# Kernel optimization log

Measured on AMD Instinct MI355X. Metric: run time of the kernel, lower is better.

Reference implementation:

```python
import jax, jax.numpy as jnp
import numpy as np

B, H, W, C = 8, 64, 64, 64
DI = 2 * C   # d_inner = ssm_ratio * hidden_dim
N = 1        # ssm_d_state
K = 4        # scan directions
R = 4        # dt_rank = ceil(C/16)
EPS = 1e-5


def _ln(x, w, b):
    mu = x.mean(-1, keepdims=True)
    var = x.var(-1, keepdims=True)
    return (x - mu) / jnp.sqrt(var + EPS) * w + b


def _vss(x, p):
    (norm1_w, norm1_b, in_proj_w, conv_w, x_proj_w, dt_projs_w, dt_projs_b,
     A_logs, Ds, out_norm_w, out_norm_b, out_proj_w, norm2_w, norm2_b,
     fc1_w, fc1_b, fc2_w, fc2_b) = p
    # ---- SS2D branch (forward_type='v2') ----
    h = _ln(x, norm1_w, norm1_b)
    xz = h @ in_proj_w.T                      # (B,H,W,2*DI)
    xc, z = jnp.split(xz, 2, axis=-1)
    z = jax.nn.silu(z)
    xc = xc.transpose(0, 3, 1, 2)             # (B,DI,H,W)
    xc = jax.lax.conv_general_dilated(
        xc, conv_w, (1, 1), [(1, 1), (1, 1)], feature_group_count=DI,
        dimension_numbers=('NCHW', 'OIHW', 'NCHW'))  # depthwise 3x3, no bias
    xc = jax.nn.silu(xc)
    L = H * W
    # CrossScan: row-major, col-major, and their reverses
    x0 = xc.reshape(B, DI, L)
    x1 = xc.transpose(0, 1, 3, 2).reshape(B, DI, L)
    xs = jnp.stack([x0, x1, x0[..., ::-1], x1[..., ::-1]], axis=1)  # (B,K,DI,L)
    x_dbl = jnp.einsum('bkdl,kcd->bkcl', xs, x_proj_w)
    dts, Bs, Cs = x_dbl[:, :, :R], x_dbl[:, :, R:R + N], x_dbl[:, :, R + N:]
    delta = jax.nn.softplus(jnp.einsum('bkrl,kdr->bkdl', dts, dt_projs_w)
                            + dt_projs_b[None, :, :, None])          # (B,K,DI,L)
    A = -jnp.exp(A_logs).reshape(K, DI, N)
    # diagonal linear recurrence h_t = a_t*h_{t-1} + b_t via associative scan
    a = jnp.exp(delta[..., None] * A[None, :, :, None, :])           # (B,K,DI,L,N)
    b = delta[..., None] * Bs.transpose(0, 1, 3, 2)[:, :, None] * xs[..., None]
    def comb(c1, c2):
        a1, b1 = c1
        a2, b2 = c2
        return a1 * a2, b1 * a2 + b2
    _, hst = jax.lax.associative_scan(comb, (a, b), axis=3)          # (B,K,DI,L,N)
    ys = jnp.einsum('bkdln,bknl->bkdl', hst, Cs) \
         + Ds.reshape(K, DI)[None, :, :, None] * xs
    # CrossMerge
    ys = ys[:, :2] + ys[:, 2:, :, ::-1]
    y = ys[:, 0] + ys[:, 1].reshape(B, DI, W, H).transpose(0, 1, 3, 2).reshape(B, DI, L)
    y = y.transpose(0, 2, 1).reshape(B, H, W, DI)
    y = _ln(y, out_norm_w, out_norm_b)
    y = (y * z) @ out_proj_w.T
    x = x + y
    # ---- MLP branch ----
    h2 = _ln(x, norm2_w, norm2_b)
    h2 = jax.nn.gelu(h2 @ fc1_w.T + fc1_b, approximate=False)
    return x + (h2 @ fc2_w.T + fc2_b)


def setup_inputs():
    key = jax.random.key(0)
    ks = jax.random.split(key, 16)
    g = lambda i, shape, s=0.02: jax.random.normal(ks[i], shape, jnp.float32) * s
    return {
        'mag': jax.random.normal(ks[0], (B, H, W, C), jnp.float32),
        'phase': jax.random.normal(ks[1], (B, H, W, C), jnp.float32),
        'norm1_w': jnp.ones((2, C)), 'norm1_b': jnp.zeros((2, C)),
        'in_proj_w': g(2, (2, 2 * DI, C)),
        'conv_w': g(3, (2, DI, 1, 3, 3), 0.1),
        'x_proj_w': g(4, (2, K, R + 2 * N, DI)),
        'dt_projs_w': g(5, (2, K, DI, R), 0.1),
        'dt_projs_b': g(6, (2, K, DI), 0.1),
        'A_logs': g(7, (2, K * DI, N), 1.0),
        'Ds': jnp.ones((2, K * DI)),
        'out_norm_w': jnp.ones((2, DI)), 'out_norm_b': jnp.zeros((2, DI)),
        'out_proj_w': g(8, (2, C, DI)),
        'norm2_w': jnp.ones((2, C)), 'norm2_b': jnp.zeros((2, C)),
        'fc1_w': g(9, (2, 4 * C, C)), 'fc1_b': jnp.zeros((2, 4 * C)),
        'fc2_w': g(10, (2, C, 4 * C)), 'fc2_b': jnp.zeros((2, C)),
    }


def reference(mag, phase, norm1_w, norm1_b, in_proj_w, conv_w, x_proj_w,
              dt_projs_w, dt_projs_b, A_logs, Ds, out_norm_w, out_norm_b,
              out_proj_w, norm2_w, norm2_b, fc1_w, fc1_b, fc2_w, fc2_b):
    params = (norm1_w, norm1_b, in_proj_w, conv_w, x_proj_w, dt_projs_w,
              dt_projs_b, A_logs, Ds, out_norm_w, out_norm_b, out_proj_w,
              norm2_w, norm2_b, fc1_w, fc1_b, fc2_w, fc2_b)
    outs = jax.vmap(_vss)(jnp.stack([mag, phase]), params)  # branch dim = 2
    s = outs[0] + outs[1]
    return (s, s)
```

## Files before the change

kernel.cpp:

```cpp
#include <hip/hip_runtime.h>
#include <math.h>

#define LL   4096
#define DI   128
#define CC   64
#define BB   8
#define KK   4
#define LB   32768
#define NPIX 2097152
#define EPSF 1e-5f

#define OFF_XCIN   ((size_t)0)
#define OFF_XCONV  ((size_t)4194304)
#define OFF_XCONVT ((size_t)8388608)
#define OFF_Z      ((size_t)12582912)
#define OFF_Y      ((size_t)16777216)
#define OFF_YT     ((size_t)20971520)
#define OFF_XDBL   ((size_t)25165824)
#define ISTRIDE    ((size_t)25952256)
#define OFF_YCOMBT OFF_XCIN
#define OFF_XNEW   OFF_YT
#define OFF_SB     OFF_Y

typedef short v8s __attribute__((ext_vector_type(8)));
typedef float v4f __attribute__((ext_vector_type(4)));

__device__ __forceinline__ float fexp_(float x){ return __expf(x); }
__device__ __forceinline__ float silu_(float x){ return __fdividef(x, 1.f+__expf(-x)); }
__device__ __forceinline__ float softplusf_(float x){
  return fmaxf(x,0.f) + __logf(1.f + __expf(-fabsf(x)));
}
__device__ __forceinline__ float geluf_(float x){ return 0.5f*x*(1.f+erff(x*0.70710678118f)); }
__device__ __forceinline__ short bf16_(float x){
  unsigned u = __float_as_uint(x);
  u += 0x7FFF + ((u>>16)&1);
  return (short)(u>>16);
}
__device__ __forceinline__ float bf2f_(short s){
  return __uint_as_float(((unsigned)(unsigned short)s)<<16);
}

#define LD16(dst, ptr) { const float4* p4_=(const float4*)(ptr);                 \
  float4 v0_=p4_[0], v1_=p4_[1], v2_=p4_[2], v3_=p4_[3];                         \
  dst[0]=v0_.x; dst[1]=v0_.y; dst[2]=v0_.z; dst[3]=v0_.w;                        \
  dst[4]=v1_.x; dst[5]=v1_.y; dst[6]=v1_.z; dst[7]=v1_.w;                        \
  dst[8]=v2_.x; dst[9]=v2_.y; dst[10]=v2_.z; dst[11]=v2_.w;                      \
  dst[12]=v3_.x; dst[13]=v3_.y; dst[14]=v3_.z; dst[15]=v3_.w; }
#define LD16H(dst, ptr) { const v8s* p8_=(const v8s*)(ptr);                      \
  v8s a0_=p8_[0], a1_=p8_[1];                                                    \
  _Pragma("unroll") for(int e_=0;e_<8;++e_){ dst[e_]=bf2f_(a0_[e_]);             \
                                             dst[8+e_]=bf2f_(a1_[e_]); } }
#define LD16HR(dst, ptr) { const v8s* p8_=(const v8s*)(ptr);                     \
  v8s a0_=p8_[0], a1_=p8_[1];                                                    \
  _Pragma("unroll") for(int e_=0;e_<8;++e_){ dst[15-e_]=bf2f_(a0_[e_]);          \
                                             dst[7-e_]=bf2f_(a1_[e_]); } }
#define ST16H(ptr, srcv) { v8s o0_, o1_;                                         \
  _Pragma("unroll") for(int e_=0;e_<8;++e_){ o0_[e_]=bf16_(srcv[e_]);            \
                                             o1_[e_]=bf16_(srcv[8+e_]); }        \
  ((v8s*)(ptr))[0]=o0_; ((v8s*)(ptr))[1]=o1_; }

__global__ __launch_bounds__(256) void k1_ln_inproj(
    const float* __restrict__ xmag, const float* __restrict__ xph,
    const float* __restrict__ n1w_, const float* __restrict__ n1b_,
    const float* __restrict__ ipw_, float* __restrict__ ws)
{
  const int i = blockIdx.y;
  const float* xin = i ? xph : xmag;
  const float* n1w = n1w_ + i*CC;
  const float* n1b = n1b_ + i*CC;
  const float* ipw = ipw_ + i*2*DI*CC;
  float* base = ws + (size_t)i*ISTRIDE;
  const int t = threadIdx.x, lane = t & 63;
  const int wv = __builtin_amdgcn_readfirstlane(t >> 6);
  const int m = lane & 15, quad = lane >> 4;
  const int p0 = blockIdx.x*64;
  const int b = p0 >> 12, l0 = p0 & (LL-1);

  __shared__ short hlds[64*72];
  __shared__ short w1lds[128*72];
  __shared__ float outs[128*68];

  {
    float hn[CC];
    const float* xr = xin + (size_t)(p0 + lane)*CC;
    LD16(hn, xr); LD16((hn+16), xr+16); LD16((hn+32), xr+32); LD16((hn+48), xr+48);
    float s1=0.f, s2=0.f;
    #pragma unroll
    for(int c=0;c<CC;++c){ s1 += hn[c]; s2 += hn[c]*hn[c]; }
    const float mu = s1*(1.f/CC);
    const float rs = rsqrtf(s2*(1.f/CC) - mu*mu + EPSF);
    if(wv==0){
      #pragma unroll
      for(int q=0;q<8;++q){
        v8s s;
        #pragma unroll
        for(int e=0;e<8;++e){
          const int c = q*8+e;
          s[e] = bf16_((hn[c]-mu)*rs*n1w[c] + n1b[c]);
        }
        *(v8s*)&hlds[lane*72 + q*8] = s;
      }
    }
  }

  for(int h=0; h<2; ++h){
    if(h) __syncthreads();
    {
      const int jl = t >> 1, hc = (t & 1)*32;
      const float* src = ipw + (size_t)(h*128 + jl)*64 + hc;
      #pragma unroll
      for(int q=0;q<4;++q){
        const float4 fa = ((const float4*)src)[q*2];
        const float4 fb = ((const float4*)src)[q*2+1];
        v8s s;
        s[0]=bf16_(fa.x); s[1]=bf16_(fa.y); s[2]=bf16_(fa.z); s[3]=bf16_(fa.w);
        s[4]=bf16_(fb.x); s[5]=bf16_(fb.y); s[6]=bf16_(fb.z); s[7]=bf16_(fb.w);
        *(v8s*)&w1lds[jl*72 + hc + q*8] = s;
      }
    }
    __syncthreads();
    #pragma unroll 2
    for(int nt=0; nt<8; ++nt){
      v4f acc = (v4f){0.f,0.f,0.f,0.f};
      #pragma unroll
      for(int ks=0; ks<2; ++ks){
        const v8s a = *(const v8s*)&hlds[(wv*16 + m)*72 + ks*32 + quad*8];
        const v8s bb = *(const v8s*)&w1lds[(nt*16 + m)*72 + ks*32 + quad*8];
        acc = __builtin_amdgcn_mfma_f32_16x16x32_bf16(a, bb, acc, 0, 0, 0);
      }
      *(float4*)&outs[(nt*16 + m)*68 + wv*16 + quad*4] =
          make_float4(acc[0], acc[1], acc[2], acc[3]);
    }
    __syncthreads();
    const int jl = t >> 1, hc = (t & 1)*32;
    if(h==0){
      short* xcb = (short*)(base + OFF_XCIN) + (size_t)b*DI*LL + (size_t)jl*LL + l0 + hc;
      const float* so = &outs[jl*68 + hc];
      ST16H(xcb, so);
      ST16H(xcb+16, (so+16));
    } else {
      short* zr = (short*)(base + OFF_Z) + (size_t)jl*LB + p0 + hc;
      float tmp[32];
      #pragma unroll
      for(int e=0;e<32;++e) tmp[e] = silu_(outs[jl*68 + hc + e]);
      ST16H(zr, tmp);
      ST16H(zr+16, (tmp+16));
    }
  }
}

__global__ __launch_bounds__(256) void k2_dwconv(
    const float* __restrict__ cw_, float* __restrict__ ws)
{
  const int i = blockIdx.y;
  const int bd = blockIdx.x;
  const int d = bd & (DI-1);
  const float* cw = cw_ + i*DI*9 + d*9;
  const short* xcin = (const short*)(ws + (size_t)i*ISTRIDE + OFF_XCIN) + (size_t)bd*LL;
  short* xconv  = (short*)(ws + (size_t)i*ISTRIDE + OFF_XCONV ) + (size_t)bd*LL;
  short* xconvT = (short*)(ws + (size_t)i*ISTRIDE + OFF_XCONVT) + (size_t)bd*LL;
  __shared__ float tin[64*65];
  __shared__ float tout[64*65];
  const int t = threadIdx.x;
  float w9[9];
  #pragma unroll
  for(int q=0;q<9;++q) w9[q] = cw[q];
  for(int idx=t; idx<4096; idx+=256)
    tin[(idx>>6)*65 + (idx&63)] = bf2f_(xcin[idx]);
  __syncthreads();
  const int w = t & 63, hb = (t>>6)*16;
  #pragma unroll
  for(int r=0;r<16;++r){
    const int h = hb + r;
    float acc = 0.f;
    #pragma unroll
    for(int dy=0;dy<3;++dy){
      const int hh = h + dy - 1;
      if(hh>=0 && hh<64){
        #pragma unroll
        for(int dx=0;dx<3;++dx){
          const int ww = w + dx - 1;
          if(ww>=0 && ww<64) acc += tin[hh*65+ww]*w9[dy*3+dx];
        }
      }
    }
    const float o = silu_(acc);
    tout[h*65+w] = o;
    xconv[h*64+w] = bf16_(o);
  }
  __syncthreads();
  const int hcol = t & 63, wb = (t>>6)*16;
  #pragma unroll
  for(int r=0;r<16;++r){
    const int wp = wb + r;
    xconvT[wp*64 + hcol] = bf16_(tout[hcol*65 + wp]);
  }
}

__global__ __launch_bounds__(256) void k3a_xproj(
    const float* __restrict__ xpw_, float* __restrict__ ws)
{
  const int i = blockIdx.z;
  const int b = blockIdx.y >> 1;
  const int kp = blockIdx.y & 1;
  const int l = blockIdx.x*256 + threadIdx.x;
  const short* src = (const short*)(ws + (size_t)i*ISTRIDE + (kp? OFF_XCONVT : OFF_XCONV))
                     + (size_t)b*DI*LL;
  const float* xpwF = xpw_ + i*KK*6*DI + kp*6*DI;
  const float* xpwB = xpw_ + i*KK*6*DI + (kp+2)*6*DI;
  float accF[6] = {0,0,0,0,0,0};
  float accB[6] = {0,0,0,0,0,0};
  for(int d=0; d<DI; ++d){
    const float xv = bf2f_(src[(size_t)d*LL + l]);
    #pragma unroll
    for(int c=0;c<6;++c){
      accF[c] += xv * xpwF[c*DI + d];
      accB[c] += xv * xpwB[c*DI + d];
    }
  }
  short* xdF = (short*)(ws + (size_t)i*ISTRIDE + OFF_XDBL) + (size_t)(b*KK+kp  )*6*LL;
  short* xdB = (short*)(ws + (size_t)i*ISTRIDE + OFF_XDBL) + (size_t)(b*KK+kp+2)*6*LL;
  #pragma unroll
  for(int c=0;c<6;++c) xdF[(size_t)c*LL + l] = bf16_(accF[c]);
  #pragma unroll
  for(int c=0;c<6;++c) xdB[(size_t)c*LL + (LL-1-l)] = bf16_(accB[c]);
}

__global__ __launch_bounds__(256,3) void k3b_scan(
    const float* __restrict__ dtw_, const float* __restrict__ dtb_,
    const float* __restrict__ alog_, const float* __restrict__ Ds_,
    float* __restrict__ ws)
{
  const int gid = blockIdx.x;
  const int i = blockIdx.y;
  const int d  = gid & (DI-1);
  const int b  = gid >> 7;
  const int t = threadIdx.x, lane = t & 63, wv = t >> 6;
  float* base = ws + (size_t)i*ISTRIDE;
  const int l0 = t*16;
  const int s0 = LL - 16 - l0;

  __shared__ float tile[64*65];
  __shared__ float wAg[4], wBg[4], vAg[4], vBg[4];

  #pragma unroll 1
  for(int kp=0; kp<2; ++kp){
    const short* src = (const short*)(base + (kp? OFF_XCONVT : OFF_XCONV)) + (size_t)(b*DI+d)*LL;
    const short* xdF = (const short*)(base + OFF_XDBL) + (size_t)(b*KK+kp  )*6*LL;
    const short* xdB = (const short*)(base + OFF_XDBL) + (size_t)(b*KK+kp+2)*6*LL;
    const int kdF = kp*DI + d, kdB = (kp+2)*DI + d;
    const float4 wF = ((const float4*)dtw_)[i*KK*DI + kdF];
    const float4 wB = ((const float4*)dtw_)[i*KK*DI + kdB];
    const float biasF = dtb_[i*KK*DI + kdF], biasB = dtb_[i*KK*DI + kdB];
    const float AvF = -fexp_(alog_[i*KK*DI + kdF]);
    const float AvB = -fexp_(alog_[i*KK*DI + kdB]);
    const float Dsum = Ds_[i*KK*DI + kdF] + Ds_[i*KK*DI + kdB];

    float vX[16], aF[16], bF[16], aB[16], bB[16];
    float fA = 1.f, fB = 0.f, gA = 1.f, gB = 0.f;
    LD16H(vX, src + l0);

    {
      float pre[16], r0[16];
      LD16H(r0, xdF + 0*LL + l0);
      #pragma unroll
      for(int j=0;j<16;++j) pre[j] = biasF + wF.x*r0[j];
      LD16H(r0, xdF + 1*LL + l0);
      #pragma unroll
      for(int j=0;j<16;++j) pre[j] += wF.y*r0[j];
      LD16H(r0, xdF + 2*LL + l0);
      #pragma unroll
      for(int j=0;j<16;++j) pre[j] += wF.z*r0[j];
      LD16H(r0, xdF + 3*LL + l0);
      #pragma unroll
      for(int j=0;j<16;++j) pre[j] += wF.w*r0[j];
      LD16H(r0, xdF + 4*LL + l0);
      #pragma unroll
      for(int j=0;j<16;++j){
        const float delta = softplusf_(pre[j]);
        aF[j] = fexp_(delta*AvF);
        bF[j] = delta*r0[j]*vX[j];
        fB = fB*aF[j] + bF[j];
        fA *= aF[j];
      }
    }
    {
      float pre[16], r0[16];
      LD16HR(r0, xdB + 0*LL + s0);
      #pragma unroll
      for(int j=0;j<16;++j) pre[j] = biasB + wB.x*r0[j];
      LD16HR(r0, xdB + 1*LL + s0);
      #pragma unroll
      for(int j=0;j<16;++j) pre[j] += wB.y*r0[j];
      LD16HR(r0, xdB + 2*LL + s0);
      #pragma unroll
      for(int j=0;j<16;++j) pre[j] += wB.z*r0[j];
      LD16HR(r0, xdB + 3*LL + s0);
      #pragma unroll
      for(int j=0;j<16;++j) pre[j] += wB.w*r0[j];
      LD16HR(r0, xdB + 4*LL + s0);
      #pragma unroll
      for(int j=15;j>=0;--j){
        const float delta = softplusf_(pre[j]);
        aB[j] = fexp_(delta*AvB);
        bB[j] = delta*r0[j]*vX[j];
        gB = gB*aB[j] + bB[j];
        gA *= aB[j];
      }
    }

    #pragma unroll
    for(int off=1; off<64; off<<=1){
      const float aL = __shfl_up(fA, off);
      const float bL = __shfl_up(fB, off);
      if(lane >= off){ fB = bL*fA + fB; fA = aL*fA; }
    }
    float pA = __shfl_up(fA, 1), pB = __shfl_up(fB, 1);
    if(lane==0){ pA=1.f; pB=0.f; }
    #pragma unroll
    for(int off=1; off<64; off<<=1){
      const float aR = __shfl_down(gA, off);
      const float bR = __shfl_down(gB, off);
      if(lane + off < 64){ gB = gA*bR + gB; gA = gA*aR; }
    }
    float qA = __shfl_down(gA, 1), qB = __shfl_down(gB, 1);
    if(lane==63){ qA=1.f; qB=0.f; }

    if(kp) __syncthreads();
    if(lane==63){ wAg[wv]=fA; wBg[wv]=fB; }
    if(lane==0){ vAg[wv]=gA; vBg[wv]=gB; }
    __syncthreads();
    float eB=0.f;
    for(int u=0; u<wv; ++u){ eB = wAg[u]*eB + wBg[u]; }
    float rB=0.f;
    for(int u=3; u>wv; --u){ rB = vAg[u]*rB + vBg[u]; }

    float hf = pA*eB + pB;
    float hb = qA*rB + qB;

    float out[16], cc[16];
    LD16H(cc, xdF + 5*LL + l0);
    #pragma unroll
    for(int j=0;j<16;++j){
      hf = aF[j]*hf + bF[j];
      out[j] = hf*cc[j] + Dsum*vX[j];
    }
    LD16HR(cc, xdB + 5*LL + s0);
    #pragma unroll
    for(int j=15;j>=0;--j){
      hb = aB[j]*hb + bB[j];
      out[j] += hb*cc[j];
    }

    if(kp==0){
      #pragma unroll
      for(int j=0;j<16;++j){
        const int l = l0 + j;
        tile[(l>>6)*65 + (l&63)] = out[j];
      }
    } else {
      #pragma unroll
      for(int j=0;j<16;++j){
        const int q = l0 + j;
        tile[(q&63)*65 + (q>>6)] += out[j];
      }
    }
  }

  __syncthreads();
  {
    short* ycT = (short*)(base + OFF_YCOMBT);
    float o[16];
    #pragma unroll
    for(int j=0;j<16;++j)
      o[j] = tile[(t>>2)*65 + (t&3)*16 + j];
    ST16H(ycT + (size_t)d*LB + b*LL + l0, o);
  }
}

__global__ __launch_bounds__(256) void k4a_proj(
    const float* __restrict__ xmag, const float* __restrict__ xph,
    const float* __restrict__ onw_, const float* __restrict__ onb_,
    const float* __restrict__ opw_, float* __restrict__ ws)
{
  const int i = blockIdx.y;
  const float* xin = i ? xph : xmag;
  const float* onw = onw_ + i*DI;
  const float* onb = onb_ + i*DI;
  const float* opw = opw_ + i*CC*DI;
  float* base = ws + (size_t)i*ISTRIDE;
  const short* ycT = (const short*)(base + OFF_YCOMBT);
  const short* zT  = (const short*)(base + OFF_Z);
  const int t = threadIdx.x, lane = t & 63;
  const int wv = __builtin_amdgcn_readfirstlane(t >> 6);
  const int m = lane & 15, quad = lane >> 4;
  const int p0 = blockIdx.x*64;
  const int p = p0 + lane;

  __shared__ short ynlds[64*136];
  __shared__ short wlds[64*136];
  __shared__ float st[64][9];

  float yv[32];
  float s1=0.f, s2=0.f;
  #pragma unroll 8
  for(int c=0;c<32;++c){
    const float v = bf2f_(ycT[(size_t)(wv*32+c)*LB + p]);
    yv[c]=v; s1+=v; s2+=v*v;
  }
  st[lane][wv*2]=s1; st[lane][wv*2+1]=s2;
  __syncthreads();
  const float S1 = st[lane][0]+st[lane][2]+st[lane][4]+st[lane][6];
  const float S2 = st[lane][1]+st[lane][3]+st[lane][5]+st[lane][7];
  const float mu = S1*(1.f/DI);
  const float rs = rsqrtf(S2*(1.f/DI) - mu*mu + EPSF);
  #pragma unroll
  for(int cq=0;cq<8;++cq){
    short4 s4;
    #pragma unroll
    for(int e=0;e<4;++e){
      const int c = cq*4+e;
      const int d = wv*32 + c;
      ((short*)&s4)[e] = bf16_(((yv[c]-mu)*rs*onw[d] + onb[d]) * bf2f_(zT[(size_t)d*LB + p]));
    }
    *(short4*)&ynlds[lane*136 + wv*32 + cq*4] = s4;
  }
  {
    const int ol = t >> 2, seg = (t & 3)*32;
    const float* src = opw + (size_t)ol*DI + seg;
    #pragma unroll
    for(int q=0;q<4;++q){
      const float4 fa = ((const float4*)src)[q*2];
      const float4 fb = ((const float4*)src)[q*2+1];
      v8s s;
      s[0]=bf16_(fa.x); s[1]=bf16_(fa.y); s[2]=bf16_(fa.z); s[3]=bf16_(fa.w);
      s[4]=bf16_(fb.x); s[5]=bf16_(fb.y); s[6]=bf16_(fb.z); s[7]=bf16_(fb.w);
      *(v8s*)&wlds[ol*136 + seg + q*8] = s;
    }
  }
  __syncthreads();

  v4f accs[4];
  #pragma unroll
  for(int nt=0; nt<4; ++nt){
    v4f acc = (v4f){0.f,0.f,0.f,0.f};
    #pragma unroll
    for(int ks=0; ks<4; ++ks){
      const v8s a = *(const v8s*)&ynlds[(wv*16 + m)*136 + ks*32 + quad*8];
      const v8s b = *(const v8s*)&wlds[(nt*16 + m)*136 + ks*32 + quad*8];
      acc = __builtin_amdgcn_mfma_f32_16x16x32_bf16(a, b, acc, 0, 0, 0);
    }
    accs[nt] = acc;
  }
  short* xnew = (short*)(base + OFF_XNEW);
  #pragma unroll
  for(int nt=0; nt<4; ++nt){
    #pragma unroll
    for(int r=0;r<4;++r){
      const int pp = p0 + wv*16 + quad*4 + r;
      const int o = nt*16 + m;
      xnew[(size_t)pp*CC + o] = bf16_(accs[nt][r] + xin[(size_t)pp*CC + o]);
    }
  }
}

__global__ __launch_bounds__(256) void k4b_mlp(
    const float* __restrict__ n2w_, const float* __restrict__ n2b_,
    const float* __restrict__ f1w_, const float* __restrict__ f1b_,
    const float* __restrict__ f2w_, const float* __restrict__ f2b_,
    float* __restrict__ ws)
{
  const int i = blockIdx.y;
  const float* n2w = n2w_ + i*CC;
  const float* n2b = n2b_ + i*CC;
  const float* f1w = f1w_ + i*256*64;
  const float* f1b = f1b_ + i*256;
  const float* f2w = f2w_ + i*64*256;
  const float* f2b = f2b_ + i*CC;
  float* base = ws + (size_t)i*ISTRIDE;
  const short* xnew = (const short*)(base + OFF_XNEW);
  const int t = threadIdx.x, lane = t & 63;
  const int wv = __builtin_amdgcn_readfirstlane(t >> 6);
  const int m = lane & 15, quad = lane >> 4;
  const int p0 = blockIdx.x*64;

  __shared__ short hlds[64*72];
  __shared__ short w1lds[128*72];
  __shared__ short glds[64*136];
  __shared__ short w2lds[64*136];

  {
    float h2[64];
    const short* xr = xnew + (size_t)(p0 + lane)*CC;
    LD16H(h2, xr); LD16H((h2+16), xr+16); LD16H((h2+32), xr+32); LD16H((h2+48), xr+48);
    float s1=0.f, s2=0.f;
    #pragma unroll
    for(int c=0;c<CC;++c){ s1 += h2[c]; s2 += h2[c]*h2[c]; }
    const float mu = s1*(1.f/CC);
    const float rs = rsqrtf(s2*(1.f/CC) - mu*mu + EPSF);
    if(wv==0){
      #pragma unroll
      for(int q=0;q<8;++q){
        v8s s;
        #pragma unroll
        for(int e=0;e<8;++e){
          const int c = q*8+e;
          s[e] = bf16_((h2[c]-mu)*rs*n2w[c] + n2b[c]);
        }
        *(v8s*)&hlds[lane*72 + q*8] = s;
      }
    }
  }

  v4f acc2[4];
  #pragma unroll
  for(int n=0;n<4;++n) acc2[n] = (v4f){0.f,0.f,0.f,0.f};

  for(int h=0; h<2; ++h){
    if(h) __syncthreads();
    {
      const int jl = t >> 1, hc = (t & 1)*32;
      const float* src = f1w + (size_t)(h*128 + jl)*64 + hc;
      #pragma unroll
      for(int q=0;q<4;++q){
        const float4 fa = ((const float4*)src)[q*2];
        const float4 fb = ((const float4*)src)[q*2+1];
        v8s s;
        s[0]=bf16_(fa.x); s[1]=bf16_(fa.y); s[2]=bf16_(fa.z); s[3]=bf16_(fa.w);
        s[4]=bf16_(fb.x); s[5]=bf16_(fb.y); s[6]=bf16_(fb.z); s[7]=bf16_(fb.w);
        *(v8s*)&w1lds[jl*72 + hc + q*8] = s;
      }
    }
    {
      const int ol = t >> 2, seg = (t & 3)*32;
      const float* src = f2w + (size_t)ol*256 + h*128 + seg;
      #pragma unroll
      for(int q=0;q<4;++q){
        const float4 fa = ((const float4*)src)[q*2];
        const float4 fb = ((const float4*)src)[q*2+1];
        v8s s;
        s[0]=bf16_(fa.x); s[1]=bf16_(fa.y); s[2]=bf16_(fa.z); s[3]=bf16_(fa.w);
        s[4]=bf16_(fb.x); s[5]=bf16_(fb.y); s[6]=bf16_(fb.z); s[7]=bf16_(fb.w);
        *(v8s*)&w2lds[ol*136 + seg + q*8] = s;
      }
    }
    __syncthreads();
    #pragma unroll 2
    for(int nt=0; nt<8; ++nt){
      v4f acc = (v4f){0.f,0.f,0.f,0.f};
      #pragma unroll
      for(int ks=0; ks<2; ++ks){
        const v8s a = *(const v8s*)&hlds[(wv*16 + m)*72 + ks*32 + quad*8];
        const v8s b = *(const v8s*)&w1lds[(nt*16 + m)*72 + ks*32 + quad*8];
        acc = __builtin_amdgcn_mfma_f32_16x16x32_bf16(a, b, acc, 0, 0, 0);
      }
      const float bj = f1b[h*128 + nt*16 + m];
      #pragma unroll
      for(int r=0;r<4;++r){
        glds[(wv*16 + quad*4 + r)*136 + nt*16 + m] = bf16_(geluf_(acc[r] + bj));
      }
    }
    #pragma unroll
    for(int nt=0; nt<4; ++nt){
      v4f acc = acc2[nt];
      #pragma unroll
      for(int ks=0; ks<4; ++ks){
        const v8s a = *(const v8s*)&glds[(wv*16 + m)*136 + ks*32 + quad*8];
        const v8s b = *(const v8s*)&w2lds[(nt*16 + m)*136 + ks*32 + quad*8];
        acc = __builtin_amdgcn_mfma_f32_16x16x32_bf16(a, b, acc, 0, 0, 0);
      }
      acc2[nt] = acc;
    }
  }

  short* sb = (short*)(base + OFF_SB);
  #pragma unroll
  for(int nt=0; nt<4; ++nt){
    const float bo = f2b[nt*16 + m];
    #pragma unroll
    for(int r=0;r<4;++r){
      const int p = p0 + wv*16 + quad*4 + r;
      const int o = nt*16 + m;
      sb[(size_t)p*CC + o] = bf16_(acc2[nt][r] + bo + bf2f_(xnew[(size_t)p*CC + o]));
    }
  }
}

__global__ __launch_bounds__(256) void k5_final(
    const float* __restrict__ ws, float* __restrict__ out)
{
  const int idx = blockIdx.x*256 + threadIdx.x;
  const v8s a = ((const v8s*)(ws + OFF_SB))[idx];
  const v8s b = ((const v8s*)(ws + ISTRIDE + OFF_SB))[idx];
  float4 v0, v1;
  v0.x = bf2f_(a[0])+bf2f_(b[0]); v0.y = bf2f_(a[1])+bf2f_(b[1]);
  v0.z = bf2f_(a[2])+bf2f_(b[2]); v0.w = bf2f_(a[3])+bf2f_(b[3]);
  v1.x = bf2f_(a[4])+bf2f_(b[4]); v1.y = bf2f_(a[5])+bf2f_(b[5]);
  v1.z = bf2f_(a[6])+bf2f_(b[6]); v1.w = bf2f_(a[7])+bf2f_(b[7]);
  ((float4*)out)[idx*2]   = v0;
  ((float4*)out)[idx*2+1] = v1;
  ((float4*)out)[NPIX/4 + idx*2]   = v0;
  ((float4*)out)[NPIX/4 + idx*2+1] = v1;
}

extern "C" void kernel_launch(void* const* d_in, const int* in_sizes, int n_in,
                              void* d_out, int out_size, void* d_ws, size_t ws_size,
                              hipStream_t stream)
{
  const float* mag  = (const float*)d_in[0];
  const float* ph   = (const float*)d_in[1];
  const float* n1w  = (const float*)d_in[2];
  const float* n1b  = (const float*)d_in[3];
  const float* ipw  = (const float*)d_in[4];
  const float* cw   = (const float*)d_in[5];
  const float* xpw  = (const float*)d_in[6];
  const float* dtw  = (const float*)d_in[7];
  const float* dtb  = (const float*)d_in[8];
  const float* alog = (const float*)d_in[9];
  const float* Ds   = (const float*)d_in[10];
  const float* onw  = (const float*)d_in[11];
  const float* onb  = (const float*)d_in[12];
  const float* opw  = (const float*)d_in[13];
  const float* n2w  = (const float*)d_in[14];
  const float* n2b  = (const float*)d_in[15];
  const float* f1w  = (const float*)d_in[16];
  const float* f1b  = (const float*)d_in[17];
  const float* f2w  = (const float*)d_in[18];
  const float* f2b  = (const float*)d_in[19];
  float* ws = (float*)d_ws;
  float* out = (float*)d_out;

  k1_ln_inproj<<<dim3(512,2),  256, 0, stream>>>(mag, ph, n1w, n1b, ipw, ws);
  k2_dwconv   <<<dim3(1024,2), 256, 0, stream>>>(cw, ws);
  k3a_xproj   <<<dim3(16,16,2),256, 0, stream>>>(xpw, ws);
  k3b_scan    <<<dim3(1024,2), 256, 0, stream>>>(dtw, dtb, alog, Ds, ws);
  k4a_proj    <<<dim3(512,2),  256, 0, stream>>>(mag, ph, onw, onb, opw, ws);
  k4b_mlp     <<<dim3(512,2),  256, 0, stream>>>(n2w, n2b, f1w, f1b, f2w, f2b, ws);
  k5_final    <<<dim3(1024),   256, 0, stream>>>(ws, out);
}
```

Measured before the change: 282.9 us.

## Fuse out-proj, MLP and branch sum into one kernel; pre-convert weights to bf16

Merges the out-projection, residual, LayerNorm2, MLP and final branch summation into a single kernel that loops over both branches per pixel tile and writes the output directly. This removes the xnew and sb intermediate round-trips through global memory and two kernel launches. A new prep kernel converts the weights to bf16 once per call, so the GEMM kernels copy bf16 weights straight into LDS instead of converting them in every block. The trade-off is half as many blocks in the fused kernel (512 instead of 1024), each doing serial work for two branches, which may reduce parallelism. The residual is also kept in fp32 rather than rounded to bf16, a small change in numerics.

```diff
diff --git a/kernel.cpp b/kernel.cpp
--- a/kernel.cpp
+++ b/kernel.cpp
@@ -19,8 +19,12 @@
 #define OFF_XDBL   ((size_t)25165824)
 #define ISTRIDE    ((size_t)25952256)
 #define OFF_YCOMBT OFF_XCIN
-#define OFF_XNEW   OFF_YT
-#define OFF_SB     OFF_Y
+#define OFF_WB     (OFF_XDBL + (size_t)393216)
+#define WB_IPW 0
+#define WB_OPW 16384
+#define WB_F1W 24576
+#define WB_F2W 40960
+#define WB_TOT 57344
 
 typedef short v8s __attribute__((ext_vector_type(8)));
 typedef float v4f __attribute__((ext_vector_type(4)));
@@ -59,17 +63,37 @@
                                              o1_[e_]=bf16_(srcv[8+e_]); }        \
   ((v8s*)(ptr))[0]=o0_; ((v8s*)(ptr))[1]=o1_; }
 
+__global__ __launch_bounds__(256) void kw_prep(
+    const float* __restrict__ ipw_, const float* __restrict__ opw_,
+    const float* __restrict__ f1w_, const float* __restrict__ f2w_,
+    float* __restrict__ ws)
+{
+  const int i = blockIdx.y;
+  short* wb = (short*)(ws + (size_t)i*ISTRIDE + OFF_WB);
+  const int e0 = blockIdx.x*1024 + threadIdx.x;
+  #pragma unroll
+  for(int k=0;k<4;++k){
+    const int e = e0 + k*256;
+    float v;
+    if(e < WB_OPW)      v = ipw_[(size_t)i*16384 + e];
+    else if(e < WB_F1W) v = opw_[(size_t)i*8192  + (e - WB_OPW)];
+    else if(e < WB_F2W) v = f1w_[(size_t)i*16384 + (e - WB_F1W)];
+    else                v = f2w_[(size_t)i*16384 + (e - WB_F2W)];
+    wb[e] = bf16_(v);
+  }
+}
+
 __global__ __launch_bounds__(256) void k1_ln_inproj(
     const float* __restrict__ xmag, const float* __restrict__ xph,
     const float* __restrict__ n1w_, const float* __restrict__ n1b_,
-    const float* __restrict__ ipw_, float* __restrict__ ws)
+    float* __restrict__ ws)
 {
   const int i = blockIdx.y;
   const float* xin = i ? xph : xmag;
   const float* n1w = n1w_ + i*CC;
   const float* n1b = n1b_ + i*CC;
-  const float* ipw = ipw_ + i*2*DI*CC;
   float* base = ws + (size_t)i*ISTRIDE;
+  const short* wb_ipw = (const short*)(base + OFF_WB) + WB_IPW;
   const int t = threadIdx.x, lane = t & 63;
   const int wv = __builtin_amdgcn_readfirstlane(t >> 6);
   const int m = lane & 15, quad = lane >> 4;
@@ -107,16 +131,10 @@
     if(h) __syncthreads();
     {
       const int jl = t >> 1, hc = (t & 1)*32;
-      const float* src = ipw + (size_t)(h*128 + jl)*64 + hc;
-      #pragma unroll
-      for(int q=0;q<4;++q){
-        const float4 fa = ((const float4*)src)[q*2];
-        const float4 fb = ((const float4*)src)[q*2+1];
-        v8s s;
-        s[0]=bf16_(fa.x); s[1]=bf16_(fa.y); s[2]=bf16_(fa.z); s[3]=bf16_(fa.w);
-        s[4]=bf16_(fb.x); s[5]=bf16_(fb.y); s[6]=bf16_(fb.z); s[7]=bf16_(fb.w);
-        *(v8s*)&w1lds[jl*72 + hc + q*8] = s;
-      }
+      const short* src = wb_ipw + (size_t)(h*128 + jl)*64 + hc;
+      #pragma unroll
+      for(int q=0;q<4;++q)
+        *(v8s*)&w1lds[jl*72 + hc + q*8] = ((const v8s*)src)[q];
     }
     __syncthreads();
     #pragma unroll 2
@@ -378,229 +396,205 @@
   }
 }
 
-__global__ __launch_bounds__(256) void k4a_proj(
+__global__ __launch_bounds__(256) void k4_fused(
     const float* __restrict__ xmag, const float* __restrict__ xph,
     const float* __restrict__ onw_, const float* __restrict__ onb_,
-    const float* __restrict__ opw_, float* __restrict__ ws)
+    const float* __restrict__ n2w_, const float* __restrict__ n2b_,
+    const float* __restrict__ f1b_, const float* __restrict__ f2b_,
+    float* __restrict__ ws, float* __restrict__ out)
 {
-  const int i = blockIdx.y;
-  const float* xin = i ? xph : xmag;
-  const float* onw = onw_ + i*DI;
-  const float* onb = onb_ + i*DI;
-  const float* opw = opw_ + i*CC*DI;
-  float* base = ws + (size_t)i*ISTRIDE;
-  const short* ycT = (const short*)(base + OFF_YCOMBT);
-  const short* zT  = (const short*)(base + OFF_Z);
   const int t = threadIdx.x, lane = t & 63;
   const int wv = __builtin_amdgcn_readfirstlane(t >> 6);
   const int m = lane & 15, quad = lane >> 4;
   const int p0 = blockIdx.x*64;
   const int p = p0 + lane;
 
-  __shared__ short ynlds[64*136];
-  __shared__ short wlds[64*136];
-  __shared__ float st[64][9];
-
-  float yv[32];
-  float s1=0.f, s2=0.f;
-  #pragma unroll 8
-  for(int c=0;c<32;++c){
-    const float v = bf2f_(ycT[(size_t)(wv*32+c)*LB + p]);
-    yv[c]=v; s1+=v; s2+=v*v;
-  }
-  st[lane][wv*2]=s1; st[lane][wv*2+1]=s2;
-  __syncthreads();
-  const float S1 = st[lane][0]+st[lane][2]+st[lane][4]+st[lane][6];
-  const float S2 = st[lane][1]+st[lane][3]+st[lane][5]+st[lane][7];
-  const float mu = S1*(1.f/DI);
-  const float rs = rsqrtf(S2*(1.f/DI) - mu*mu + EPSF);
-  #pragma unroll
-  for(int cq=0;cq<8;++cq){
-    short4 s4;
-    #pragma unroll
-    for(int e=0;e<4;++e){
-      const int c = cq*4+e;
-      const int d = wv*32 + c;
-      ((short*)&s4)[e] = bf16_(((yv[c]-mu)*rs*onw[d] + onb[d]) * bf2f_(zT[(size_t)d*LB + p]));
-    }
-    *(short4*)&ynlds[lane*136 + wv*32 + cq*4] = s4;
-  }
-  {
-    const int ol = t >> 2, seg = (t & 3)*32;
-    const float* src = opw + (size_t)ol*DI + seg;
-    #pragma unroll
-    for(int q=0;q<4;++q){
-      const float4 fa = ((const float4*)src)[q*2];
-      const float4 fb = ((const float4*)src)[q*2+1];
-      v8s s;
-      s[0]=bf16_(fa.x); s[1]=bf16_(fa.y); s[2]=bf16_(fa.z); s[3]=bf16_(fa.w);
-      s[4]=bf16_(fb.x); s[5]=bf16_(fb.y); s[6]=bf16_(fb.z); s[7]=bf16_(fb.w);
-      *(v8s*)&wlds[ol*136 + seg + q*8] = s;
-    }
-  }
-  __syncthreads();
-
-  v4f accs[4];
-  #pragma unroll
-  for(int nt=0; nt<4; ++nt){
-    v4f acc = (v4f){0.f,0.f,0.f,0.f};
-    #pragma unroll
-    for(int ks=0; ks<4; ++ks){
-      const v8s a = *(const v8s*)&ynlds[(wv*16 + m)*136 + ks*32 + quad*8];
-      const v8s b = *(const v8s*)&wlds[(nt*16 + m)*136 + ks*32 + quad*8];
-      acc = __builtin_amdgcn_mfma_f32_16x16x32_bf16(a, b, acc, 0, 0, 0);
-    }
-    accs[nt] = acc;
-  }
-  short* xnew = (short*)(base + OFF_XNEW);
+  __shared__ union {
+    struct {
+      float st[64][9];
+      short ynlds[64*136];
+      short wlds[64*136];
+    } a;
+    struct {
+      short hlds[64*72];
+      short w1lds[128*72];
+      short glds[64*136];
+      short w2lds[64*136];
+    } b;
+  } U;
+  __shared__ short xnlds[64*72];
+
+  float outsum[16];
+  #pragma unroll
+  for(int e=0;e<16;++e) outsum[e]=0.f;
+
+  #pragma unroll 1
+  for(int i=0;i<2;++i){
+    float* base = ws + (size_t)i*ISTRIDE;
+    const short* ycT = (const short*)(base + OFF_YCOMBT);
+    const short* zT  = (const short*)(base + OFF_Z);
+    const short* wb  = (const short*)(base + OFF_WB);
+    const float* xin = i ? xph : xmag;
+    const float* onw = onw_ + i*DI;
+    const float* onb = onb_ + i*DI;
+    const float* n2w = n2w_ + i*CC;
+    const float* n2b = n2b_ + i*CC;
+    const float* f1b = f1b_ + i*256;
+    const float* f2b = f2b_ + i*CC;
+
+    if(i) __syncthreads();
+
+    float yv[32];
+    float s1=0.f, s2=0.f;
+    #pragma unroll 8
+    for(int c=0;c<32;++c){
+      const float v = bf2f_(ycT[(size_t)(wv*32+c)*LB + p]);
+      yv[c]=v; s1+=v; s2+=v*v;
+    }
+    U.a.st[lane][wv*2]=s1; U.a.st[lane][wv*2+1]=s2;
+    __syncthreads();
+    const float S1 = U.a.st[lane][0]+U.a.st[lane][2]+U.a.st[lane][4]+U.a.st[lane][6];
+    const float S2 = U.a.st[lane][1]+U.a.st[lane][3]+U.a.st[lane][5]+U.a.st[lane][7];
+    const float mu = S1*(1.f/DI);
+    const float rs = rsqrtf(S2*(1.f/DI) - mu*mu + EPSF);
+    #pragma unroll
+    for(int cq=0;cq<8;++cq){
+      short4 s4;
+      #pragma unroll
+      for(int e=0;e<4;++e){
+        const int c = cq*4+e;
+        const int d = wv*32 + c;
+        ((short*)&s4)[e] = bf16_(((yv[c]-mu)*rs*onw[d] + onb[d]) * bf2f_(zT[(size_t)d*LB + p]));
+      }
+      *(short4*)&U.a.ynlds[lane*136 + wv*32 + cq*4] = s4;
+    }
+    {
+      const int ol = t >> 2, seg = (t & 3)*32;
+      const short* src = wb + WB_OPW + (size_t)ol*DI + seg;
+      #pragma unroll
+      for(int q=0;q<4;++q)
+        *(v8s*)&U.a.wlds[ol*136 + seg + q*8] = ((const v8s*)src)[q];
+    }
+    __syncthreads();
+
+    float xres[16];
+    {
+      v4f accs[4];
+      #pragma unroll
+      for(int nt=0; nt<4; ++nt){
+        v4f acc = (v4f){0.f,0.f,0.f,0.f};
+        #pragma unroll
+        for(int ks=0; ks<4; ++ks){
+          const v8s a = *(const v8s*)&U.a.ynlds[(wv*16 + m)*136 + ks*32 + quad*8];
+          const v8s bb = *(const v8s*)&U.a.wlds[(nt*16 + m)*136 + ks*32 + quad*8];
+          acc = __builtin_amdgcn_mfma_f32_16x16x32_bf16(a, bb, acc, 0, 0, 0);
+        }
+        accs[nt] = acc;
+      }
+      #pragma unroll
+      for(int nt=0; nt<4; ++nt){
+        #pragma unroll
+        for(int r=0;r<4;++r){
+          const int pp = p0 + wv*16 + quad*4 + r;
+          const int o  = nt*16 + m;
+          const float xv = accs[nt][r] + xin[(size_t)pp*CC + o];
+          xres[nt*4+r] = xv;
+          xnlds[(wv*16 + quad*4 + r)*72 + o] = bf16_(xv);
+        }
+      }
+    }
+    __syncthreads();
+
+    if(wv==0){
+      float ssum=0.f, ssq=0.f;
+      #pragma unroll
+      for(int q=0;q<8;++q){
+        const v8s v = *(const v8s*)&xnlds[lane*72 + q*8];
+        #pragma unroll
+        for(int e=0;e<8;++e){ const float f=bf2f_(v[e]); ssum+=f; ssq+=f*f; }
+      }
+      const float mu2 = ssum*(1.f/CC);
+      const float rs2 = rsqrtf(ssq*(1.f/CC) - mu2*mu2 + EPSF);
+      #pragma unroll
+      for(int q=0;q<8;++q){
+        const v8s v = *(const v8s*)&xnlds[lane*72 + q*8];
+        v8s o8;
+        #pragma unroll
+        for(int e=0;e<8;++e){
+          const int c = q*8+e;
+          o8[e] = bf16_((bf2f_(v[e])-mu2)*rs2*n2w[c] + n2b[c]);
+        }
+        *(v8s*)&U.b.hlds[lane*72 + q*8] = o8;
+      }
+    }
+
+    v4f acc2[4];
+    #pragma unroll
+    for(int n=0;n<4;++n) acc2[n] = (v4f){0.f,0.f,0.f,0.f};
+
+    for(int h=0; h<2; ++h){
+      if(h) __syncthreads();
+      {
+        const int jl = t >> 1, hc = (t & 1)*32;
+        const short* src = wb + WB_F1W + (size_t)(h*128 + jl)*64 + hc;
+        #pragma unroll
+        for(int q=0;q<4;++q)
+          *(v8s*)&U.b.w1lds[jl*72 + hc + q*8] = ((const v8s*)src)[q];
+      }
+      {
+        const int ol = t >> 2, seg = (t & 3)*32;
+        const short* src = wb + WB_F2W + (size_t)ol*256 + h*128 + seg;
+        #pragma unroll
+        for(int q=0;q<4;++q)
+          *(v8s*)&U.b.w2lds[ol*136 + seg + q*8] = ((const v8s*)src)[q];
+      }
+      __syncthreads();
+      #pragma unroll 2
+      for(int nt=0; nt<8; ++nt){
+        v4f acc = (v4f){0.f,0.f,0.f,0.f};
+        #pragma unroll
+        for(int ks=0; ks<2; ++ks){
+          const v8s a = *(const v8s*)&U.b.hlds[(wv*16 + m)*72 + ks*32 + quad*8];
+          const v8s bb = *(const v8s*)&U.b.w1lds[(nt*16 + m)*72 + ks*32 + quad*8];
+          acc = __builtin_amdgcn_mfma_f32_16x16x32_bf16(a, bb, acc, 0, 0, 0);
+        }
+        const float bj = f1b[h*128 + nt*16 + m];
+        #pragma unroll
+        for(int r=0;r<4;++r)
+          U.b.glds[(wv*16 + quad*4 + r)*136 + nt*16 + m] = bf16_(geluf_(acc[r] + bj));
+      }
+      #pragma unroll
+      for(int nt=0; nt<4; ++nt){
+        v4f acc = acc2[nt];
+        #pragma unroll
+        for(int ks=0; ks<4; ++ks){
+          const v8s a = *(const v8s*)&U.b.glds[(wv*16 + m)*136 + ks*32 + quad*8];
+          const v8s bb = *(const v8s*)&U.b.w2lds[(nt*16 + m)*136 + ks*32 + quad*8];
+          acc = __builtin_amdgcn_mfma_f32_16x16x32_bf16(a, bb, acc, 0, 0, 0);
+        }
+        acc2[nt] = acc;
+      }
+    }
+
+    #pragma unroll
+    for(int nt=0; nt<4; ++nt){
+      const float bo = f2b[nt*16 + m];
+      #pragma unroll
+      for(int r=0;r<4;++r)
+        outsum[nt*4+r] += acc2[nt][r] + bo + xres[nt*4+r];
+    }
+  }
+
   #pragma unroll
   for(int nt=0; nt<4; ++nt){
     #pragma unroll
     for(int r=0;r<4;++r){
       const int pp = p0 + wv*16 + quad*4 + r;
-      const int o = nt*16 + m;
-      xnew[(size_t)pp*CC + o] = bf16_(accs[nt][r] + xin[(size_t)pp*CC + o]);
-    }
-  }
-}
-
-__global__ __launch_bounds__(256) void k4b_mlp(
-    const float* __restrict__ n2w_, const float* __restrict__ n2b_,
-    const float* __restrict__ f1w_, const float* __restrict__ f1b_,
-    const float* __restrict__ f2w_, const float* __restrict__ f2b_,
-    float* __restrict__ ws)
-{
-  const int i = blockIdx.y;
-  const float* n2w = n2w_ + i*CC;
-  const float* n2b = n2b_ + i*CC;
-  const float* f1w = f1w_ + i*256*64;
-  const float* f1b = f1b_ + i*256;
-  const float* f2w = f2w_ + i*64*256;
-  const float* f2b = f2b_ + i*CC;
-  float* base = ws + (size_t)i*ISTRIDE;
-  const short* xnew = (const short*)(base + OFF_XNEW);
-  const int t = threadIdx.x, lane = t & 63;
-  const int wv = __builtin_amdgcn_readfirstlane(t >> 6);
-  const int m = lane & 15, quad = lane >> 4;
-  const int p0 = blockIdx.x*64;
-
-  __shared__ short hlds[64*72];
-  __shared__ short w1lds[128*72];
-  __shared__ short glds[64*136];
-  __shared__ short w2lds[64*136];
-
-  {
-    float h2[64];
-    const short* xr = xnew + (size_t)(p0 + lane)*CC;
-    LD16H(h2, xr); LD16H((h2+16), xr+16); LD16H((h2+32), xr+32); LD16H((h2+48), xr+48);
-    float s1=0.f, s2=0.f;
-    #pragma unroll
-    for(int c=0;c<CC;++c){ s1 += h2[c]; s2 += h2[c]*h2[c]; }
-    const float mu = s1*(1.f/CC);
-    const float rs = rsqrtf(s2*(1.f/CC) - mu*mu + EPSF);
-    if(wv==0){
-      #pragma unroll
-      for(int q=0;q<8;++q){
-        v8s s;
-        #pragma unroll
-        for(int e=0;e<8;++e){
-          const int c = q*8+e;
-          s[e] = bf16_((h2[c]-mu)*rs*n2w[c] + n2b[c]);
-        }
-        *(v8s*)&hlds[lane*72 + q*8] = s;
-      }
-    }
-  }
-
-  v4f acc2[4];
-  #pragma unroll
-  for(int n=0;n<4;++n) acc2[n] = (v4f){0.f,0.f,0.f,0.f};
-
-  for(int h=0; h<2; ++h){
-    if(h) __syncthreads();
-    {
-      const int jl = t >> 1, hc = (t & 1)*32;
-      const float* src = f1w + (size_t)(h*128 + jl)*64 + hc;
-      #pragma unroll
-      for(int q=0;q<4;++q){
-        const float4 fa = ((const float4*)src)[q*2];
-        const float4 fb = ((const float4*)src)[q*2+1];
-        v8s s;
-        s[0]=bf16_(fa.x); s[1]=bf16_(fa.y); s[2]=bf16_(fa.z); s[3]=bf16_(fa.w);
-        s[4]=bf16_(fb.x); s[5]=bf16_(fb.y); s[6]=bf16_(fb.z); s[7]=bf16_(fb.w);
-        *(v8s*)&w1lds[jl*72 + hc + q*8] = s;
-      }
-    }
-    {
-      const int ol = t >> 2, seg = (t & 3)*32;
-      const float* src = f2w + (size_t)ol*256 + h*128 + seg;
-      #pragma unroll
-      for(int q=0;q<4;++q){
-        const float4 fa = ((const float4*)src)[q*2];
-        const float4 fb = ((const float4*)src)[q*2+1];
-        v8s s;
-        s[0]=bf16_(fa.x); s[1]=bf16_(fa.y); s[2]=bf16_(fa.z); s[3]=bf16_(fa.w);
-        s[4]=bf16_(fb.x); s[5]=bf16_(fb.y); s[6]=bf16_(fb.z); s[7]=bf16_(fb.w);
-        *(v8s*)&w2lds[ol*136 + seg + q*8] = s;
-      }
-    }
-    __syncthreads();
-    #pragma unroll 2
-    for(int nt=0; nt<8; ++nt){
-      v4f acc = (v4f){0.f,0.f,0.f,0.f};
-      #pragma unroll
-      for(int ks=0; ks<2; ++ks){
-        const v8s a = *(const v8s*)&hlds[(wv*16 + m)*72 + ks*32 + quad*8];
-        const v8s b = *(const v8s*)&w1lds[(nt*16 + m)*72 + ks*32 + quad*8];
-        acc = __builtin_amdgcn_mfma_f32_16x16x32_bf16(a, b, acc, 0, 0, 0);
-      }
-      const float bj = f1b[h*128 + nt*16 + m];
-      #pragma unroll
-      for(int r=0;r<4;++r){
-        glds[(wv*16 + quad*4 + r)*136 + nt*16 + m] = bf16_(geluf_(acc[r] + bj));
-      }
-    }
-    #pragma unroll
-    for(int nt=0; nt<4; ++nt){
-      v4f acc = acc2[nt];
-      #pragma unroll
-      for(int ks=0; ks<4; ++ks){
-        const v8s a = *(const v8s*)&glds[(wv*16 + m)*136 + ks*32 + quad*8];
-        const v8s b = *(const v8s*)&w2lds[(nt*16 + m)*136 + ks*32 + quad*8];
-        acc = __builtin_amdgcn_mfma_f32_16x16x32_bf16(a, b, acc, 0, 0, 0);
-      }
-      acc2[nt] = acc;
-    }
-  }
-
-  short* sb = (short*)(base + OFF_SB);
-  #pragma unroll
-  for(int nt=0; nt<4; ++nt){
-    const float bo = f2b[nt*16 + m];
-    #pragma unroll
-    for(int r=0;r<4;++r){
-      const int p = p0 + wv*16 + quad*4 + r;
-      const int o = nt*16 + m;
-      sb[(size_t)p*CC + o] = bf16_(acc2[nt][r] + bo + bf2f_(xnew[(size_t)p*CC + o]));
-    }
-  }
-}
-
-__global__ __launch_bounds__(256) void k5_final(
-    const float* __restrict__ ws, float* __restrict__ out)
-{
-  const int idx = blockIdx.x*256 + threadIdx.x;
-  const v8s a = ((const v8s*)(ws + OFF_SB))[idx];
-  const v8s b = ((const v8s*)(ws + ISTRIDE + OFF_SB))[idx];
-  float4 v0, v1;
-  v0.x = bf2f_(a[0])+bf2f_(b[0]); v0.y = bf2f_(a[1])+bf2f_(b[1]);
-  v0.z = bf2f_(a[2])+bf2f_(b[2]); v0.w = bf2f_(a[3])+bf2f_(b[3]);
-  v1.x = bf2f_(a[4])+bf2f_(b[4]); v1.y = bf2f_(a[5])+bf2f_(b[5]);
-  v1.z = bf2f_(a[6])+bf2f_(b[6]); v1.w = bf2f_(a[7])+bf2f_(b[7]);
-  ((float4*)out)[idx*2]   = v0;
-  ((float4*)out)[idx*2+1] = v1;
-  ((float4*)out)[NPIX/4 + idx*2]   = v0;
-  ((float4*)out)[NPIX/4 + idx*2+1] = v1;
+      const int o  = nt*16 + m;
+      out[(size_t)pp*CC + o] = outsum[nt*4+r];
+      out[(size_t)NPIX + (size_t)pp*CC + o] = outsum[nt*4+r];
+    }
+  }
 }
 
 extern "C" void kernel_launch(void* const* d_in, const int* in_sizes, int n_in,
@@ -630,11 +624,11 @@
   float* ws = (float*)d_ws;
   float* out = (float*)d_out;
 
-  k1_ln_inproj<<<dim3(512,2),  256, 0, stream>>>(mag, ph, n1w, n1b, ipw, ws);
+  kw_prep     <<<dim3(56,2),   256, 0, stream>>>(ipw, opw, f1w, f2w, ws);
+  k1_ln_inproj<<<dim3(512,2),  256, 0, stream>>>(mag, ph, n1w, n1b, ws);
   k2_dwconv   <<<dim3(1024,2), 256, 0, stream>>>(cw, ws);
   k3a_xproj   <<<dim3(16,16,2),256, 0, stream>>>(xpw, ws);
   k3b_scan    <<<dim3(1024,2), 256, 0, stream>>>(dtw, dtb, alog, Ds, ws);
-  k4a_proj    <<<dim3(512,2),  256, 0, stream>>>(mag, ph, onw, onb, opw, ws);
-  k4b_mlp     <<<dim3(512,2),  256, 0, stream>>>(n2w, n2b, f1w, f1b, f2w, f2b, ws);
-  k5_final    <<<dim3(1024),   256, 0, stream>>>(ws, out);
-}
+  k4_fused    <<<dim3(512),    256, 0, stream>>>(mag, ph, onw, onb, n2w, n2b,
+                                                 f1b, f2b, ws, out);
+}
```

Result: slower. 329.7 us (+16.6%).
